# Kernel optimization log

Hardware: AMD Instinct MI355X
Metric: run time of the kernel (lower is better)

Reference implementation:

```python
import jax, jax.numpy as jnp
from jax import lax
import numpy as np

B = 128      # graphs
L = 128      # nodes (tokens) per graph
N = B * L    # total nodes
E = 262144   # edges (avg degree 16)
VOCAB = 50000
EMB = 300
H = 256      # lstm hidden per direction
GCN = 512
NCLS = 2
EPS = 1e-12


def lstm_dir(x, wih, whh, b, reverse):
    # x: [B, L, EMB]; wih: [4H, EMB]; whh: [4H, H]; b: [4H]
    bsz, seq, _ = x.shape
    hdim = whh.shape[1]
    xs = jnp.einsum('ble,ge->blg', x, wih) + b  # [B, L, 4H]
    if reverse:
        xs = xs[:, ::-1]
    def step(carry, xt):
        h, c = carry
        gates = xt + h @ whh.T
        i, f, g, o = jnp.split(gates, 4, axis=-1)  # torch gate order i,f,g,o
        i = jax.nn.sigmoid(i); f = jax.nn.sigmoid(f)
        g = jnp.tanh(g); o = jax.nn.sigmoid(o)
        c = f * c + i * g
        h = o * jnp.tanh(c)
        return (h, c), h
    h0 = jnp.zeros((bsz, hdim), x.dtype)
    _, hs = lax.scan(step, (h0, h0), jnp.swapaxes(xs, 0, 1))
    hs = jnp.swapaxes(hs, 0, 1)  # [B, L, H]
    if reverse:
        hs = hs[:, ::-1]
    return hs


def sage_conv(x, src, dst, Wl, bl, Wr):
    # PyG SAGEConv(mean, normalize=True): lin_l(mean_j x_j) + lin_r(x_i), then L2-normalize
    msg = x[src]                                              # [E, d] gather
    agg = jax.ops.segment_sum(msg, dst, num_segments=x.shape[0])
    cnt = jax.ops.segment_sum(jnp.ones((src.shape[0], 1), x.dtype), dst,
                              num_segments=x.shape[0])
    agg = agg / jnp.maximum(cnt, 1.0)
    out = agg @ Wl + bl + x @ Wr
    nrm = jnp.linalg.norm(out, axis=-1, keepdims=True)
    return out / jnp.maximum(nrm, EPS)


def setup_inputs() -> dict:
    key = jax.random.key(0)
    ks = jax.random.split(key, 24)
    word_seq = jax.random.randint(ks[0], (B, L), 0, VOCAB)
    # intra-graph edges: local endpoints + graph offset
    el = jax.random.randint(ks[1], (2, E), 0, L)
    gid = jnp.repeat(jnp.arange(E // (E // B) * 0 + B), E // B)  # [E]
    edge_index = el + gid[None, :] * L
    batch = jnp.repeat(jnp.arange(B), L)
    s = 0.05
    inp = {
        'word_seq': word_seq, 'edge_index': edge_index, 'batch': batch,
        'embed_table': jax.random.normal(ks[2], (VOCAB, EMB), jnp.float32) * 0.1,
        'wih_f': jax.random.normal(ks[3], (4 * H, EMB), jnp.float32) * s,
        'whh_f': jax.random.normal(ks[4], (4 * H, H), jnp.float32) * s,
        'b_f': jax.random.normal(ks[5], (4 * H,), jnp.float32) * s,
        'wih_b': jax.random.normal(ks[6], (4 * H, EMB), jnp.float32) * s,
        'whh_b': jax.random.normal(ks[7], (4 * H, H), jnp.float32) * s,
        'b_b': jax.random.normal(ks[8], (4 * H,), jnp.float32) * s,
        'Wl1': jax.random.normal(ks[9], (2 * H, GCN), jnp.float32) * s,
        'Wr1': jax.random.normal(ks[10], (2 * H, GCN), jnp.float32) * s,
        'b1': jnp.zeros((GCN,), jnp.float32),
        'Wl2': jax.random.normal(ks[11], (GCN, 512), jnp.float32) * s,
        'Wr2': jax.random.normal(ks[12], (GCN, 512), jnp.float32) * s,
        'b2': jnp.zeros((512,), jnp.float32),
        'Wl3': jax.random.normal(ks[13], (512, 512), jnp.float32) * s,
        'Wr3': jax.random.normal(ks[14], (512, 512), jnp.float32) * s,
        'b3': jnp.zeros((512,), jnp.float32),
        'Wlin': jax.random.normal(ks[15], (512, NCLS), jnp.float32) * s,
        'blin': jnp.zeros((NCLS,), jnp.float32),
    }
    return inp


def reference(word_seq, edge_index, batch, embed_table,
              wih_f, whh_f, b_f, wih_b, whh_b, b_b,
              Wl1, Wr1, b1, Wl2, Wr2, b2, Wl3, Wr3, b3, Wlin, blin):
    # embedding (frozen) over padded per-graph sequences; uniform lengths -> plain reshape
    xe = embed_table[word_seq]                       # [B, L, EMB]
    hf = lstm_dir(xe, wih_f, whh_f, b_f, reverse=False)
    hb = lstm_dir(xe, wih_b, whh_b, b_b, reverse=True)
    x = jnp.concatenate([hf, hb], axis=-1).reshape(N, 2 * H)  # node features
    src, dst = edge_index[0], edge_index[1]
    x = jax.nn.relu(sage_conv(x, src, dst, Wl1, b1, Wr1))
    x = jax.nn.relu(sage_conv(x, src, dst, Wl2, b2, Wr2))
    x = jax.nn.relu(sage_conv(x, src, dst, Wl3, b3, Wr3))
    # global mean pool over graphs
    s = jax.ops.segment_sum(x, batch, num_segments=B)
    c = jax.ops.segment_sum(jnp.ones((N, 1), x.dtype), batch, num_segments=B)
    pooled = s / jnp.maximum(c, 1.0)
    return pooled @ Wlin + blin                      # [B, NCLS]
```

## Files before the change

kernel.cpp:

```cpp
#include <hip/hip_runtime.h>
#include <math.h>

#define NN   16384
#define EE   262144

typedef __attribute__((ext_vector_type(8))) short  short8v;
typedef __attribute__((ext_vector_type(4))) float  f32x4;

__device__ inline unsigned short f2bf(float f) {
    union { float f; unsigned u; } v; v.f = f;
    unsigned r = v.u + 0x7fff + ((v.u >> 16) & 1);
    return (unsigned short)(r >> 16);
}
__device__ inline float bf2f(unsigned short b) {
    unsigned u = ((unsigned)b) << 16;
    union { unsigned u; float f; } v; v.u = u; return v.f;
}
__device__ inline float sigm_f(float x) { return 1.f / (1.f + __expf(-x)); }
__device__ inline float tanh_f(float x) {
    x = fminf(15.f, fmaxf(-15.f, x));
    float e = __expf(2.f * x);
    return (e - 1.f) / (e + 1.f);
}
__device__ inline int gate_orig2(int np) {
    int Q = np >> 8, wv = (np >> 5) & 7, tile = (np >> 4) & 1, tc = np & 15;
    int g = tile * 2 + (tc >> 3);
    int j = Q * 64 + wv * 8 + (tc & 7);
    return g * 256 + j;
}

__device__ __forceinline__ void gload16(const unsigned short* g, unsigned short* l) {
    __builtin_amdgcn_global_load_lds(
        (const __attribute__((address_space(1))) void*)g,
        (__attribute__((address_space(3))) void*)l,
        16, 0, 0);
}

__global__ void k_init(unsigned long long* __restrict__ hx, int* __restrict__ deg,
                       int* __restrict__ fill) {
    int i = blockIdx.x * 256 + threadIdx.x;
    if (i < 65536) hx[i] = 0ull;
    if (i < NN) { deg[i] = 0; fill[i] = 0; }
}

__global__ void k_embed_bf(const int* __restrict__ wseq, const float* __restrict__ tab,
                           unsigned short* __restrict__ xeb) {
    int i = blockIdx.x * 256 + threadIdx.x;
    if (i >= NN * 320) return;
    int row = i / 320, k = i - row * 320;
    float f = (k < 300) ? tab[wseq[row] * 300 + k] : 0.f;
    xeb[i] = f2bf(f);
}

__global__ void k_cvt_wih(const float* __restrict__ wih, unsigned short* __restrict__ wt) {
    int i = blockIdx.x * 256 + threadIdx.x;
    if (i >= 1024 * 320) return;
    int np = i / 320, k = i - np * 320;
    wt[i] = f2bf(k < 300 ? wih[gate_orig2(np) * 300 + k] : 0.f);
}
__global__ void k_cvt_whh(const float* __restrict__ whh, unsigned short* __restrict__ wp) {
    int i = blockIdx.x * 256 + threadIdx.x;
    if (i >= 1024 * 256) return;
    int np = i >> 8, k = i & 255;
    wp[i] = f2bf(whh[gate_orig2(np) * 256 + k]);
}
__global__ void k_permb(const float* __restrict__ b, float* __restrict__ pb) {
    int i = blockIdx.x * 256 + threadIdx.x;
    if (i < 1024) pb[i] = b[gate_orig2(i)];
}
__global__ void k_cvt_wcat(const float* __restrict__ Wl, const float* __restrict__ Wr,
                           unsigned short* __restrict__ wc) {
    int i = blockIdx.x * 256 + threadIdx.x;
    if (i >= 512 * 1024) return;
    int n = i >> 10, k = i & 1023;
    float f = (k < 512) ? Wl[k * 512 + n] : Wr[(k - 512) * 512 + n];
    wc[i] = f2bf(f);
}

__global__ __launch_bounds__(256)
void k_mgemm(const unsigned short* __restrict__ A, const unsigned short* __restrict__ Bt,
             const float* __restrict__ bias, float* __restrict__ C, int N, int Ka)
{
    __shared__ __align__(16) unsigned short As[128 * 32];
    __shared__ __align__(16) unsigned short Bs[128 * 32];
    const int tid = threadIdx.x;
    const int m0 = blockIdx.x << 7, n0 = blockIdx.y << 7;
    const int w = tid >> 6, lane = tid & 63;
    const int wr = w >> 1, wc = w & 1;
    const int lr = lane & 15, lhi = lane >> 4;
    const int rA  = w * 16 + (lane >> 2);
    const int kcA = (lane & 3) * 8;

    const unsigned short* gA0 = A  + (size_t)(m0 + rA) * Ka + kcA;
    const unsigned short* gA1 = gA0 + (size_t)64 * Ka;
    const unsigned short* gB0 = Bt + (size_t)(n0 + rA) * Ka + kcA;
    const unsigned short* gB1 = gB0 + (size_t)64 * Ka;
    unsigned short* lA0 = As + w * 512;
    unsigned short* lA1 = As + 64 * 32 + w * 512;
    unsigned short* lB0 = Bs + w * 512;
    unsigned short* lB1 = Bs + 64 * 32 + w * 512;

    f32x4 acc[4][4] = {};

    for (int k0 = 0; k0 < Ka; k0 += 32) {
        gload16(gA0 + k0, lA0);
        gload16(gA1 + k0, lA1);
        gload16(gB0 + k0, lB0);
        gload16(gB1 + k0, lB1);
        asm volatile("s_waitcnt vmcnt(0)" ::: "memory");
        __syncthreads();
        short8v af[4], bf[4];
        #pragma unroll
        for (int i = 0; i < 4; ++i)
            af[i] = *(const short8v*)&As[(wr * 64 + i * 16 + lr) * 32 + lhi * 8];
        #pragma unroll
        for (int j = 0; j < 4; ++j)
            bf[j] = *(const short8v*)&Bs[(wc * 64 + j * 16 + lr) * 32 + lhi * 8];
        #pragma unroll
        for (int i = 0; i < 4; ++i)
            #pragma unroll
            for (int j = 0; j < 4; ++j)
                acc[i][j] = __builtin_amdgcn_mfma_f32_16x16x32_bf16(af[i], bf[j], acc[i][j], 0, 0, 0);
        __syncthreads();
    }
    #pragma unroll
    for (int i = 0; i < 4; ++i) {
        int row = m0 + wr * 64 + i * 16 + lhi * 4;
        #pragma unroll
        for (int j = 0; j < 4; ++j) {
            int col = n0 + wc * 64 + j * 16 + lr;
            float bv = bias[col];
            #pragma unroll
            for (int r = 0; r < 4; ++r)
                C[(row + r) * N + col] = acc[i][j][r] + bv;
        }
    }
}

__global__ __launch_bounds__(512, 2)
void k_lstm(const float* __restrict__ xs_f, const float* __restrict__ xs_b,
            const unsigned short* __restrict__ whhp_f, const unsigned short* __restrict__ whhp_b,
            unsigned short* __restrict__ xout, unsigned long long* __restrict__ hx)
{
    const int tid  = threadIdx.x;
    const int wv   = tid >> 6, lane = tid & 63;
    const int lr16 = lane & 15, lh = lane >> 4;
    const int b3   = (lane >> 3) & 1, lr3 = lane & 7;
    const int wgid = blockIdx.x;
    const int dir  = wgid >> 5;
    const int bs   = (wgid >> 2) & 7;
    const int Q    = wgid & 3;
    const int b0   = bs * 16;
    const float* xs = dir ? xs_b : xs_f;
    const unsigned short* whhp = dir ? whhp_b : whhp_f;

    const int ncol0 = Q * 256 + wv * 32 + lr16;
    short8v wf[2][8];
    #pragma unroll
    for (int tt = 0; tt < 2; ++tt)
        #pragma unroll
        for (int ks = 0; ks < 8; ++ks)
            wf[tt][ks] = *(const short8v*)(whhp
                + (size_t)(ncol0 + tt * 16) * 256 + ks * 32 + lh * 8);

    __shared__ unsigned short At[2][16 * 256];

    const int grpbase = (dir * 8 + bs) * 4 * 1024;
    unsigned long long* hx_own = hx + grpbase + Q * 1024;

    const int jmine = Q * 64 + wv * 8 + lr3;
    const int rowb  = 4 * lh;
    const int myr0  = rowb + 2 * b3;
    const int up_jl = (tid >> 6) * 8 + (tid & 7);
    const int up_r0 = 2 * ((tid >> 3) & 7);

    float c0 = 0.f, c1 = 0.f;
    float xv0[4], xv1[4];
    {
        const int l0 = dir ? 127 : 0;
        #pragma unroll
        for (int r = 0; r < 4; ++r) {
            const float* xp = xs + ((size_t)(b0 + rowb + r) * 128 + l0) * 1024;
            xv0[r] = xp[ncol0];
            xv1[r] = xp[ncol0 + 16];
        }
    }

    for (int t = 0; t < 128; ++t) {
        const int l = dir ? (127 - t) : t;
        f32x4 acc0 = {}, acc1 = {};
        if (t > 0) {
            const char* Ab = (const char*)&At[(t - 1) & 1][0];
            #pragma unroll
            for (int ks = 0; ks < 8; ++ks) {
                int off = (lr16 * 512 + ks * 64 + lh * 16) ^ ((lr16 & 7) << 4);
                short8v a = *(const short8v*)(Ab + off);
                acc0 = __builtin_amdgcn_mfma_f32_16x16x32_bf16(a, wf[0][ks], acc0, 0, 0, 0);
                acc1 = __builtin_amdgcn_mfma_f32_16x16x32_bf16(a, wf[1][ks], acc1, 0, 0, 0);
            }
        }
        #pragma unroll
        for (int r = 0; r < 4; ++r) { acc0[r] += xv0[r]; acc1[r] += xv1[r]; }
        float z0 = b3 ? acc0[0] : acc0[2];
        float z1 = b3 ? acc0[1] : acc0[3];
        float z2 = b3 ? acc1[0] : acc1[2];
        float z3 = b3 ? acc1[1] : acc1[3];
        float y0 = __shfl_xor(z0, 8);
        float y1 = __shfl_xor(z1, 8);
        float y2 = __shfl_xor(z2, 8);
        float y3 = __shfl_xor(z3, 8);
        float iv0 = b3 ? y0 : acc0[0], iv1 = b3 ? y1 : acc0[1];
        float fv0 = b3 ? acc0[2] : y0, fv1 = b3 ? acc0[3] : y1;
        float gv0 = b3 ? y2 : acc1[0], gv1 = b3 ? y3 : acc1[1];
        float ov0 = b3 ? acc1[2] : y2, ov1 = b3 ? acc1[3] : y3;
        iv0 = sigm_f(iv0); fv0 = sigm_f(fv0); gv0 = tanh_f(gv0); ov0 = sigm_f(ov0);
        c0 = fv0 * c0 + iv0 * gv0;
        float h0 = ov0 * tanh_f(c0);
        iv1 = sigm_f(iv1); fv1 = sigm_f(fv1); gv1 = tanh_f(gv1); ov1 = sigm_f(ov1);
        c1 = fv1 * c1 + iv1 * gv1;
        float h1 = ov1 * tanh_f(c1);
        unsigned short hb0 = f2bf(h0), hb1 = f2bf(h1);
        xout[((size_t)(b0 + myr0)     * 128 + l) * 512 + dir * 256 + jmine] = hb0;
        xout[((size_t)(b0 + myr0 + 1) * 128 + l) * 512 + dir * 256 + jmine] = hb1;

        if (t < 127) {
            const int p = t & 1;
            char* Aw = (char*)&At[p][0];
            {
                int r0_ = myr0, r1_ = myr0 + 1;
                *(unsigned short*)(Aw + ((r0_ * 512 + 2 * jmine) ^ ((r0_ & 7) << 4))) = hb0;
                *(unsigned short*)(Aw + ((r1_ * 512 + 2 * jmine) ^ ((r1_ & 7) << 4))) = hb1;
            }
            const unsigned tg = (unsigned)(t + 1);
            unsigned long long w = ((unsigned long long)tg << 32)
                                 | ((unsigned)hb0 | ((unsigned)hb1 << 16));
            __hip_atomic_store(hx_own + p * 512 + tid, w,
                               __ATOMIC_RELAXED, __HIP_MEMORY_SCOPE_AGENT);
            const int l2 = dir ? (126 - t) : (t + 1);
            #pragma unroll
            for (int r = 0; r < 4; ++r) {
                const float* xp = xs + ((size_t)(b0 + rowb + r) * 128 + l2) * 1024;
                xv0[r] = xp[ncol0];
                xv1[r] = xp[ncol0 + 16];
            }
            const unsigned long long* pp1 = hx + grpbase + (Q ^ 1) * 1024 + p * 512 + tid;
            const unsigned long long* pp2 = hx + grpbase + (Q ^ 2) * 1024 + p * 512 + tid;
            const unsigned long long* pp3 = hx + grpbase + (Q ^ 3) * 1024 + p * 512 + tid;
            unsigned long long u1 = __hip_atomic_load(pp1, __ATOMIC_RELAXED, __HIP_MEMORY_SCOPE_AGENT);
            unsigned long long u2 = __hip_atomic_load(pp2, __ATOMIC_RELAXED, __HIP_MEMORY_SCOPE_AGENT);
            unsigned long long u3 = __hip_atomic_load(pp3, __ATOMIC_RELAXED, __HIP_MEMORY_SCOPE_AGENT);
            while ((unsigned)(u1 >> 32) != tg)
                u1 = __hip_atomic_load(pp1, __ATOMIC_RELAXED, __HIP_MEMORY_SCOPE_AGENT);
            while ((unsigned)(u2 >> 32) != tg)
                u2 = __hip_atomic_load(pp2, __ATOMIC_RELAXED, __HIP_MEMORY_SCOPE_AGENT);
            while ((unsigned)(u3 >> 32) != tg)
                u3 = __hip_atomic_load(pp3, __ATOMIC_RELAXED, __HIP_MEMORY_SCOPE_AGENT);
            {
                int ra = up_r0, rb = up_r0 + 1;
                int j1 = (Q ^ 1) * 64 + up_jl;
                int j2 = (Q ^ 2) * 64 + up_jl;
                int j3 = (Q ^ 3) * 64 + up_jl;
                *(unsigned short*)(Aw + ((ra * 512 + 2 * j1) ^ ((ra & 7) << 4))) =
                    (unsigned short)(u1 & 0xffff);
                *(unsigned short*)(Aw + ((rb * 512 + 2 * j1) ^ ((rb & 7) << 4))) =
                    (unsigned short)((u1 >> 16) & 0xffff);
                *(unsigned short*)(Aw + ((ra * 512 + 2 * j2) ^ ((ra & 7) << 4))) =
                    (unsigned short)(u2 & 0xffff);
                *(unsigned short*)(Aw + ((rb * 512 + 2 * j2) ^ ((rb & 7) << 4))) =
                    (unsigned short)((u2 >> 16) & 0xffff);
                *(unsigned short*)(Aw + ((ra * 512 + 2 * j3) ^ ((ra & 7) << 4))) =
                    (unsigned short)(u3 & 0xffff);
                *(unsigned short*)(Aw + ((rb * 512 + 2 * j3) ^ ((rb & 7) << 4))) =
                    (unsigned short)((u3 >> 16) & 0xffff);
            }
            __syncthreads();
        }
    }
}

__global__ void k_hist(const int* __restrict__ ei, int* __restrict__ deg) {
    int e = blockIdx.x * 256 + threadIdx.x;
    if (e >= EE) return;
    atomicAdd(&deg[ei[EE + e]], 1);
}

__global__ void k_scan(const int* __restrict__ deg, int* __restrict__ indptr) {
    __shared__ int sm[256];
    int tid = threadIdx.x;
    int b0 = tid * 64;
    int s = 0;
    for (int i = 0; i < 64; ++i) s += deg[b0 + i];
    sm[tid] = s;
    __syncthreads();
    for (int off = 1; off < 256; off <<= 1) {
        int v = (tid >= off) ? sm[tid - off] : 0;
        __syncthreads();
        sm[tid] += v;
        __syncthreads();
    }
    int run = sm[tid] - s;
    for (int i = 0; i < 64; ++i) { indptr[b0 + i] = run; run += deg[b0 + i]; }
    if (tid == 255) indptr[NN] = run;
}

__global__ void k_scatter(const int* __restrict__ ei, const int* __restrict__ indptr,
                          int* __restrict__ fill, int* __restrict__ cols) {
    int e = blockIdx.x * 256 + threadIdx.x;
    if (e >= EE) return;
    int d = ei[EE + e];
    int slot = atomicAdd(&fill[d], 1);
    cols[indptr[d] + slot] = ei[e];
}

__global__ __launch_bounds__(512)
void k_gather_lds(const unsigned short* __restrict__ x, const int* __restrict__ indptr,
                  const int* __restrict__ cols, unsigned short* __restrict__ catb)
{
    extern __shared__ char gsm[];
    unsigned short* Xs = (unsigned short*)gsm;
    const int tid  = threadIdx.x;
    const int g    = blockIdx.x >> 1;
    const int hf   = blockIdx.x & 1;
    const int base = g * 128;
    {
        const unsigned short* src = x + (size_t)base * 512;
        #pragma unroll
        for (int it = 0; it < 16; ++it) {
            int i = it * 512 + tid;
            int row = i >> 6, c = (i & 63) * 8;
            *(short8v*)(Xs + row * 512 + c) = *(const short8v*)(src + (size_t)row * 512 + c);
        }
    }
    __syncthreads();
    const int wv = tid >> 6, lane = tid & 63;
    for (int rr = 0; rr < 8; ++rr) {
        int node = base + hf * 64 + rr * 8 + wv;
        int s = indptr[node], e = indptr[node + 1];
        float a[8] = {};
        for (int p = s; p < e; ++p) {
            int lrow = cols[p] - base;
            short8v v = *(const short8v*)(Xs + lrow * 512 + lane * 8);
            #pragma unroll
            for (int q = 0; q < 8; ++q) a[q] += bf2f((unsigned short)v[q]);
        }
        float sc = 1.f / (float)((e - s) > 1 ? (e - s) : 1);
        unsigned short o[8];
        #pragma unroll
        for (int q = 0; q < 8; ++q) o[q] = f2bf(a[q] * sc);
        unsigned short* cp = catb + (size_t)node * 1024 + lane * 8;
        *(short8v*)cp = *(short8v*)o;
        *(short8v*)(cp + 512) = *(const short8v*)(Xs + (node - base) * 512 + lane * 8);
    }
}

__global__ __launch_bounds__(256)
void k_norm_relu_bf(const float* __restrict__ y, unsigned short* __restrict__ o)
{
    int gw = (blockIdx.x * 256 + threadIdx.x) >> 6;
    int lane = threadIdx.x & 63;
    if (gw >= NN) return;
    const float* row = y + gw * 512 + lane * 8;
    float4 v0 = *(const float4*)row;
    float4 v1 = *(const float4*)(row + 4);
    float ss = v0.x*v0.x + v0.y*v0.y + v0.z*v0.z + v0.w*v0.w
             + v1.x*v1.x + v1.y*v1.y + v1.z*v1.z + v1.w*v1.w;
    #pragma unroll
    for (int off = 32; off >= 1; off >>= 1) ss += __shfl_xor(ss, off);
    float sc = 1.f / fmaxf(sqrtf(ss), 1e-12f);
    unsigned short ob[8];
    ob[0] = f2bf(fmaxf(v0.x*sc, 0.f)); ob[1] = f2bf(fmaxf(v0.y*sc, 0.f));
    ob[2] = f2bf(fmaxf(v0.z*sc, 0.f)); ob[3] = f2bf(fmaxf(v0.w*sc, 0.f));
    ob[4] = f2bf(fmaxf(v1.x*sc, 0.f)); ob[5] = f2bf(fmaxf(v1.y*sc, 0.f));
    ob[6] = f2bf(fmaxf(v1.z*sc, 0.f)); ob[7] = f2bf(fmaxf(v1.w*sc, 0.f));
    *(short8v*)(o + gw * 512 + lane * 8) = *(short8v*)ob;
}

__global__ __launch_bounds__(256)
void k_pool_bf(const unsigned short* __restrict__ x, const float* __restrict__ Wlin,
               const float* __restrict__ blin, float* __restrict__ out)
{
    int g = blockIdx.x;
    int tid = threadIdx.x;
    const unsigned short* base = x + (size_t)g * 128 * 512;
    float a0 = 0.f, a1 = 0.f;
    for (int r = 0; r < 128; ++r) {
        unsigned v = *(const unsigned*)(base + r * 512 + 2 * tid);
        a0 += bf2f((unsigned short)(v & 0xffff));
        a1 += bf2f((unsigned short)(v >> 16));
    }
    __shared__ float pooled[512];
    pooled[2*tid]     = a0 * (1.f / 128.f);
    pooled[2*tid + 1] = a1 * (1.f / 128.f);
    __syncthreads();
    if (tid < 64) {
        float p0 = 0.f, p1 = 0.f;
        for (int k = tid; k < 512; k += 64) {
            float pv = pooled[k];
            p0 += pv * Wlin[2*k];
            p1 += pv * Wlin[2*k + 1];
        }
        #pragma unroll
        for (int off = 32; off >= 1; off >>= 1) {
            p0 += __shfl_xor(p0, off);
            p1 += __shfl_xor(p1, off);
        }
        if (tid == 0) {
            out[2*g]     = p0 + blin[0];
            out[2*g + 1] = p1 + blin[1];
        }
    }
}

extern "C" void kernel_launch(void* const* d_in, const int* in_sizes, int n_in,
                              void* d_out, int out_size, void* d_ws, size_t ws_size,
                              hipStream_t stream)
{
    (void)in_sizes; (void)n_in; (void)out_size; (void)ws_size;
    const int*   word_seq = (const int*)  d_in[0];
    const int*   ei       = (const int*)  d_in[1];
    const float* tab      = (const float*)d_in[3];
    const float* wih_f    = (const float*)d_in[4];
    const float* whh_f    = (const float*)d_in[5];
    const float* b_f      = (const float*)d_in[6];
    const float* wih_b    = (const float*)d_in[7];
    const float* whh_b    = (const float*)d_in[8];
    const float* b_b      = (const float*)d_in[9];
    const float* Wl1      = (const float*)d_in[10];
    const float* Wr1      = (const float*)d_in[11];
    const float* b1       = (const float*)d_in[12];
    const float* Wl2      = (const float*)d_in[13];
    const float* Wr2      = (const float*)d_in[14];
    const float* b2       = (const float*)d_in[15];
    const float* Wl3      = (const float*)d_in[16];
    const float* Wr3      = (const float*)d_in[17];
    const float* b3       = (const float*)d_in[18];
    const float* Wlin     = (const float*)d_in[19];
    const float* blin     = (const float*)d_in[20];
    float* out = (float*)d_out;

    char* w = (char*)d_ws;
    int*   deg    = (int*)  (w);
    int*   indptr = (int*)  (w + 65536);
    int*   fill   = (int*)  (w + 131584);
    int*   cols   = (int*)  (w + 197120);
    unsigned long long* hx = (unsigned long long*)(w + 1245696);
    unsigned short* whhp_f = (unsigned short*)(w + 1769984);
    unsigned short* whhp_b = (unsigned short*)(w + 2294272);
    float* pb_f   = (float*)(w + 2818560);
    float* pb_b   = (float*)(w + 2822656);
    unsigned short* wt_f = (unsigned short*)(w + 2826752);
    unsigned short* wt_b = (unsigned short*)(w + 3482112);
    unsigned short* wc1  = (unsigned short*)(w + 4137472);
    unsigned short* wc2  = (unsigned short*)(w + 5186048);
    unsigned short* wc3  = (unsigned short*)(w + 6234624);
    unsigned short* xeb  = (unsigned short*)(w + 7283200);
    float* xs_f   = (float*)(w + 17768960);
    float* xs_b   = (float*)(w + 84877824);
    unsigned short* x0b = (unsigned short*)(w + 151986688);
    unsigned short* catb = (unsigned short*)(w + 17768960);
    float* x1     = (float*)(w + 51323392);
    unsigned short* xb_a = (unsigned short*)(w + 84877824);
    unsigned short* xb_b = (unsigned short*)(w + 101655040);

    k_embed_bf<<<20480, 256, 0, stream>>>(word_seq, tab, xeb);
    k_cvt_wih<<<1280, 256, 0, stream>>>(wih_f, wt_f);
    k_cvt_wih<<<1280, 256, 0, stream>>>(wih_b, wt_b);
    k_cvt_whh<<<1024, 256, 0, stream>>>(whh_f, whhp_f);
    k_cvt_whh<<<1024, 256, 0, stream>>>(whh_b, whhp_b);
    k_permb<<<4, 256, 0, stream>>>(b_f, pb_f);
    k_permb<<<4, 256, 0, stream>>>(b_b, pb_b);
    k_cvt_wcat<<<2048, 256, 0, stream>>>(Wl1, Wr1, wc1);
    k_cvt_wcat<<<2048, 256, 0, stream>>>(Wl2, Wr2, wc2);
    k_cvt_wcat<<<2048, 256, 0, stream>>>(Wl3, Wr3, wc3);

    k_init<<<256, 256, 0, stream>>>(hx, deg, fill);
    k_hist<<<1024, 256, 0, stream>>>(ei, deg);
    k_scan<<<1, 256, 0, stream>>>(deg, indptr);
    k_scatter<<<1024, 256, 0, stream>>>(ei, indptr, fill, cols);

    k_mgemm<<<dim3(128, 8), 256, 0, stream>>>(xeb, wt_f, pb_f, xs_f, 1024, 320);
    k_mgemm<<<dim3(128, 8), 256, 0, stream>>>(xeb, wt_b, pb_b, xs_b, 1024, 320);

    k_lstm<<<64, 512, 0, stream>>>(xs_f, xs_b, whhp_f, whhp_b, x0b, hx);

    k_gather_lds<<<256, 512, 131072, stream>>>(x0b, indptr, cols, catb);
    k_mgemm<<<dim3(128, 4), 256, 0, stream>>>(catb, wc1, b1, x1, 512, 1024);
    k_norm_relu_bf<<<4096, 256, 0, stream>>>(x1, xb_a);
    k_gather_lds<<<256, 512, 131072, stream>>>(xb_a, indptr, cols, catb);
    k_mgemm<<<dim3(128, 4), 256, 0, stream>>>(catb, wc2, b2, x1, 512, 1024);
    k_norm_relu_bf<<<4096, 256, 0, stream>>>(x1, xb_b);
    k_gather_lds<<<256, 512, 131072, stream>>>(xb_b, indptr, cols, catb);
    k_mgemm<<<dim3(128, 4), 256, 0, stream>>>(catb, wc3, b3, x1, 512, 1024);
    k_norm_relu_bf<<<4096, 256, 0, stream>>>(x1, xb_a);

    k_pool_bf<<<128, 256, 0, stream>>>(xb_a, Wlin, blin, out);
}
```

Measured before the change: 649.9 us.

## Interleave two batch slices per LSTM workgroup to hide cross-block exchange latency

Each LSTM workgroup now handles two 16-row batch slices instead of one, so the grid is halved from 64 to 32 blocks. The slices run staggered, and one slice's cross-quarter hidden-state exchange through global atomics overlaps with the other slice's MFMA and gate math. The goal is to hide the spin-wait and global-memory round-trip latency that dominates each recurrent step. In exchange, half as many CUs are used and per-block serial work doubles, so the gain depends on how much of each step was latency rather than compute.

Measured after the change: 810.9 us. 24.8% more time.

```diff
diff --git a/kernel.cpp b/kernel.cpp
--- a/kernel.cpp
+++ b/kernel.cpp
@@ -147,10 +147,10 @@
     const int lr16 = lane & 15, lh = lane >> 4;
     const int b3   = (lane >> 3) & 1, lr3 = lane & 7;
     const int wgid = blockIdx.x;
-    const int dir  = wgid >> 5;
-    const int bs   = (wgid >> 2) & 7;
+    const int dir  = wgid >> 4;
+    const int bp   = (wgid >> 2) & 3;
     const int Q    = wgid & 3;
-    const int b0   = bs * 16;
+    const int b0s0 = bp * 32, b0s1 = bp * 32 + 16;
     const float* xs = dir ? xs_b : xs_f;
     const unsigned short* whhp = dir ? whhp_b : whhp_f;
 
@@ -163,118 +163,200 @@
             wf[tt][ks] = *(const short8v*)(whhp
                 + (size_t)(ncol0 + tt * 16) * 256 + ks * 32 + lh * 8);
 
-    __shared__ unsigned short At[2][16 * 256];
-
-    const int grpbase = (dir * 8 + bs) * 4 * 1024;
-    unsigned long long* hx_own = hx + grpbase + Q * 1024;
+    __shared__ unsigned short At[2][2][16 * 256];
+
+    const int grpQ = (dir * 4 + bp) * 4;
+    unsigned long long* hx_own = hx + (size_t)(grpQ + Q) * 2048;
+    const unsigned long long* hx_p1 = hx + (size_t)(grpQ + (Q ^ 1)) * 2048;
+    const unsigned long long* hx_p2 = hx + (size_t)(grpQ + (Q ^ 2)) * 2048;
+    const unsigned long long* hx_p3 = hx + (size_t)(grpQ + (Q ^ 3)) * 2048;
 
     const int jmine = Q * 64 + wv * 8 + lr3;
     const int rowb  = 4 * lh;
     const int myr0  = rowb + 2 * b3;
     const int up_jl = (tid >> 6) * 8 + (tid & 7);
     const int up_r0 = 2 * ((tid >> 3) & 7);
-
-    float c0 = 0.f, c1 = 0.f;
-    float xv0[4], xv1[4];
+    const int j1 = (Q ^ 1) * 64 + up_jl;
+    const int j2 = (Q ^ 2) * 64 + up_jl;
+    const int j3 = (Q ^ 3) * 64 + up_jl;
+
+    float c0a = 0.f, c1a = 0.f;
+    float c0b = 0.f, c1b = 0.f;
+    float xva0[4], xva1[4], xvb0[4], xvb1[4];
     {
         const int l0 = dir ? 127 : 0;
         #pragma unroll
         for (int r = 0; r < 4; ++r) {
-            const float* xp = xs + ((size_t)(b0 + rowb + r) * 128 + l0) * 1024;
-            xv0[r] = xp[ncol0];
-            xv1[r] = xp[ncol0 + 16];
+            const float* xpa = xs + ((size_t)(b0s0 + rowb + r) * 128 + l0) * 1024;
+            const float* xpb = xs + ((size_t)(b0s1 + rowb + r) * 128 + l0) * 1024;
+            xva0[r] = xpa[ncol0]; xva1[r] = xpa[ncol0 + 16];
+            xvb0[r] = xpb[ncol0]; xvb1[r] = xpb[ncol0 + 16];
         }
     }
 
     for (int t = 0; t < 128; ++t) {
-        const int l = dir ? (127 - t) : t;
-        f32x4 acc0 = {}, acc1 = {};
-        if (t > 0) {
-            const char* Ab = (const char*)&At[(t - 1) & 1][0];
+        const int l  = dir ? (127 - t) : t;
+        const int l2 = dir ? (126 - t) : (t + 1);
+        const int p  = t & 1, q = p ^ 1;
+        const unsigned tg  = (unsigned)t;
+        const unsigned tg1 = (unsigned)(t + 1);
+
+        {
+            f32x4 acc0 = {}, acc1 = {};
+            if (t > 0) {
+                const char* Ab = (const char*)&At[0][q][0];
+                #pragma unroll
+                for (int ks = 0; ks < 8; ++ks) {
+                    int off = (lr16 * 512 + ks * 64 + lh * 16) ^ ((lr16 & 7) << 4);
+                    short8v a = *(const short8v*)(Ab + off);
+                    acc0 = __builtin_amdgcn_mfma_f32_16x16x32_bf16(a, wf[0][ks], acc0, 0, 0, 0);
+                    acc1 = __builtin_amdgcn_mfma_f32_16x16x32_bf16(a, wf[1][ks], acc1, 0, 0, 0);
+                }
+            }
             #pragma unroll
-            for (int ks = 0; ks < 8; ++ks) {
-                int off = (lr16 * 512 + ks * 64 + lh * 16) ^ ((lr16 & 7) << 4);
-                short8v a = *(const short8v*)(Ab + off);
-                acc0 = __builtin_amdgcn_mfma_f32_16x16x32_bf16(a, wf[0][ks], acc0, 0, 0, 0);
-                acc1 = __builtin_amdgcn_mfma_f32_16x16x32_bf16(a, wf[1][ks], acc1, 0, 0, 0);
-            }
-        }
-        #pragma unroll
-        for (int r = 0; r < 4; ++r) { acc0[r] += xv0[r]; acc1[r] += xv1[r]; }
-        float z0 = b3 ? acc0[0] : acc0[2];
-        float z1 = b3 ? acc0[1] : acc0[3];
-        float z2 = b3 ? acc1[0] : acc1[2];
-        float z3 = b3 ? acc1[1] : acc1[3];
-        float y0 = __shfl_xor(z0, 8);
-        float y1 = __shfl_xor(z1, 8);
-        float y2 = __shfl_xor(z2, 8);
-        float y3 = __shfl_xor(z3, 8);
-        float iv0 = b3 ? y0 : acc0[0], iv1 = b3 ? y1 : acc0[1];
-        float fv0 = b3 ? acc0[2] : y0, fv1 = b3 ? acc0[3] : y1;
-        float gv0 = b3 ? y2 : acc1[0], gv1 = b3 ? y3 : acc1[1];
-        float ov0 = b3 ? acc1[2] : y2, ov1 = b3 ? acc1[3] : y3;
-        iv0 = sigm_f(iv0); fv0 = sigm_f(fv0); gv0 = tanh_f(gv0); ov0 = sigm_f(ov0);
-        c0 = fv0 * c0 + iv0 * gv0;
-        float h0 = ov0 * tanh_f(c0);
-        iv1 = sigm_f(iv1); fv1 = sigm_f(fv1); gv1 = tanh_f(gv1); ov1 = sigm_f(ov1);
-        c1 = fv1 * c1 + iv1 * gv1;
-        float h1 = ov1 * tanh_f(c1);
-        unsigned short hb0 = f2bf(h0), hb1 = f2bf(h1);
-        xout[((size_t)(b0 + myr0)     * 128 + l) * 512 + dir * 256 + jmine] = hb0;
-        xout[((size_t)(b0 + myr0 + 1) * 128 + l) * 512 + dir * 256 + jmine] = hb1;
-
-        if (t < 127) {
-            const int p = t & 1;
-            char* Aw = (char*)&At[p][0];
-            {
+            for (int r = 0; r < 4; ++r) { acc0[r] += xva0[r]; acc1[r] += xva1[r]; }
+            float z0 = b3 ? acc0[0] : acc0[2];
+            float z1 = b3 ? acc0[1] : acc0[3];
+            float z2 = b3 ? acc1[0] : acc1[2];
+            float z3 = b3 ? acc1[1] : acc1[3];
+            float y0 = __shfl_xor(z0, 8);
+            float y1 = __shfl_xor(z1, 8);
+            float y2 = __shfl_xor(z2, 8);
+            float y3 = __shfl_xor(z3, 8);
+            float iv0 = b3 ? y0 : acc0[0], iv1 = b3 ? y1 : acc0[1];
+            float fv0 = b3 ? acc0[2] : y0, fv1 = b3 ? acc0[3] : y1;
+            float gv0 = b3 ? y2 : acc1[0], gv1 = b3 ? y3 : acc1[1];
+            float ov0 = b3 ? acc1[2] : y2, ov1 = b3 ? acc1[3] : y3;
+            iv0 = sigm_f(iv0); fv0 = sigm_f(fv0); gv0 = tanh_f(gv0); ov0 = sigm_f(ov0);
+            c0a = fv0 * c0a + iv0 * gv0;
+            float h0 = ov0 * tanh_f(c0a);
+            iv1 = sigm_f(iv1); fv1 = sigm_f(fv1); gv1 = tanh_f(gv1); ov1 = sigm_f(ov1);
+            c1a = fv1 * c1a + iv1 * gv1;
+            float h1 = ov1 * tanh_f(c1a);
+            unsigned short hb0 = f2bf(h0), hb1 = f2bf(h1);
+            xout[((size_t)(b0s0 + myr0)     * 128 + l) * 512 + dir * 256 + jmine] = hb0;
+            xout[((size_t)(b0s0 + myr0 + 1) * 128 + l) * 512 + dir * 256 + jmine] = hb1;
+            if (t < 127) {
+                char* Aw = (char*)&At[0][p][0];
                 int r0_ = myr0, r1_ = myr0 + 1;
                 *(unsigned short*)(Aw + ((r0_ * 512 + 2 * jmine) ^ ((r0_ & 7) << 4))) = hb0;
                 *(unsigned short*)(Aw + ((r1_ * 512 + 2 * jmine) ^ ((r1_ & 7) << 4))) = hb1;
+                unsigned long long w = ((unsigned long long)tg1 << 32)
+                                     | ((unsigned)hb0 | ((unsigned)hb1 << 16));
+                __hip_atomic_store(hx_own + (0 * 2 + p) * 512 + tid, w,
+                                   __ATOMIC_RELAXED, __HIP_MEMORY_SCOPE_AGENT);
+                #pragma unroll
+                for (int r = 0; r < 4; ++r) {
+                    const float* xp = xs + ((size_t)(b0s0 + rowb + r) * 128 + l2) * 1024;
+                    xva0[r] = xp[ncol0]; xva1[r] = xp[ncol0 + 16];
+                }
             }
-            const unsigned tg = (unsigned)(t + 1);
-            unsigned long long w = ((unsigned long long)tg << 32)
-                                 | ((unsigned)hb0 | ((unsigned)hb1 << 16));
-            __hip_atomic_store(hx_own + p * 512 + tid, w,
-                               __ATOMIC_RELAXED, __HIP_MEMORY_SCOPE_AGENT);
-            const int l2 = dir ? (126 - t) : (t + 1);
+        }
+        if (t > 0) {
+            const int so = (1 * 2 + q) * 512 + tid;
+            unsigned long long u1 = __hip_atomic_load(hx_p1 + so, __ATOMIC_RELAXED, __HIP_MEMORY_SCOPE_AGENT);
+            unsigned long long u2 = __hip_atomic_load(hx_p2 + so, __ATOMIC_RELAXED, __HIP_MEMORY_SCOPE_AGENT);
+            unsigned long long u3 = __hip_atomic_load(hx_p3 + so, __ATOMIC_RELAXED, __HIP_MEMORY_SCOPE_AGENT);
+            while ((unsigned)(u1 >> 32) != tg)
+                u1 = __hip_atomic_load(hx_p1 + so, __ATOMIC_RELAXED, __HIP_MEMORY_SCOPE_AGENT);
+            while ((unsigned)(u2 >> 32) != tg)
+                u2 = __hip_atomic_load(hx_p2 + so, __ATOMIC_RELAXED, __HIP_MEMORY_SCOPE_AGENT);
+            while ((unsigned)(u3 >> 32) != tg)
+                u3 = __hip_atomic_load(hx_p3 + so, __ATOMIC_RELAXED, __HIP_MEMORY_SCOPE_AGENT);
+            char* Aw = (char*)&At[1][q][0];
+            int ra = up_r0, rb = up_r0 + 1;
+            *(unsigned short*)(Aw + ((ra * 512 + 2 * j1) ^ ((ra & 7) << 4))) =
+                (unsigned short)(u1 & 0xffff);
+            *(unsigned short*)(Aw + ((rb * 512 + 2 * j1) ^ ((rb & 7) << 4))) =
+                (unsigned short)((u1 >> 16) & 0xffff);
+            *(unsigned short*)(Aw + ((ra * 512 + 2 * j2) ^ ((ra & 7) << 4))) =
+                (unsigned short)(u2 & 0xffff);
+            *(unsigned short*)(Aw + ((rb * 512 + 2 * j2) ^ ((rb & 7) << 4))) =
+                (unsigned short)((u2 >> 16) & 0xffff);
+            *(unsigned short*)(Aw + ((ra * 512 + 2 * j3) ^ ((ra & 7) << 4))) =
+                (unsigned short)(u3 & 0xffff);
+            *(unsigned short*)(Aw + ((rb * 512 + 2 * j3) ^ ((rb & 7) << 4))) =
+                (unsigned short)((u3 >> 16) & 0xffff);
+        }
+        __syncthreads();
+        {
+            f32x4 acc0 = {}, acc1 = {};
+            if (t > 0) {
+                const char* Ab = (const char*)&At[1][q][0];
+                #pragma unroll
+                for (int ks = 0; ks < 8; ++ks) {
+                    int off = (lr16 * 512 + ks * 64 + lh * 16) ^ ((lr16 & 7) << 4);
+                    short8v a = *(const short8v*)(Ab + off);
+                    acc0 = __builtin_amdgcn_mfma_f32_16x16x32_bf16(a, wf[0][ks], acc0, 0, 0, 0);
+                    acc1 = __builtin_amdgcn_mfma_f32_16x16x32_bf16(a, wf[1][ks], acc1, 0, 0, 0);
+                }
+            }
             #pragma unroll
-            for (int r = 0; r < 4; ++r) {
-                const float* xp = xs + ((size_t)(b0 + rowb + r) * 128 + l2) * 1024;
-                xv0[r] = xp[ncol0];
-                xv1[r] = xp[ncol0 + 16];
+            for (int r = 0; r < 4; ++r) { acc0[r] += xvb0[r]; acc1[r] += xvb1[r]; }
+            float z0 = b3 ? acc0[0] : acc0[2];
+            float z1 = b3 ? acc0[1] : acc0[3];
+            float z2 = b3 ? acc1[0] : acc1[2];
+            float z3 = b3 ? acc1[1] : acc1[3];
+            float y0 = __shfl_xor(z0, 8);
+            float y1 = __shfl_xor(z1, 8);
+            float y2 = __shfl_xor(z2, 8);
+            float y3 = __shfl_xor(z3, 8);
+            float iv0 = b3 ? y0 : acc0[0], iv1 = b3 ? y1 : acc0[1];
+            float fv0 = b3 ? acc0[2] : y0, fv1 = b3 ? acc0[3] : y1;
+            float gv0 = b3 ? y2 : acc1[0], gv1 = b3 ? y3 : acc1[1];
+            float ov0 = b3 ? acc1[2] : y2, ov1 = b3 ? acc1[3] : y3;
+            iv0 = sigm_f(iv0); fv0 = sigm_f(fv0); gv0 = tanh_f(gv0); ov0 = sigm_f(ov0);
+            c0b = fv0 * c0b + iv0 * gv0;
+            float h0 = ov0 * tanh_f(c0b);
+            iv1 = sigm_f(iv1); fv1 = sigm_f(fv1); gv1 = tanh_f(gv1); ov1 = sigm_f(ov1);
+            c1b = fv1 * c1b + iv1 * gv1;
+            float h1 = ov1 * tanh_f(c1b);
+            unsigned short hb0 = f2bf(h0), hb1 = f2bf(h1);
+            xout[((size_t)(b0s1 + myr0)     * 128 + l) * 512 + dir * 256 + jmine] = hb0;
+            xout[((size_t)(b0s1 + myr0 + 1) * 128 + l) * 512 + dir * 256 + jmine] = hb1;
+            if (t < 127) {
+                char* Aw = (char*)&At[1][p][0];
+                int r0_ = myr0, r1_ = myr0 + 1;
+                *(unsigned short*)(Aw + ((r0_ * 512 + 2 * jmine) ^ ((r0_ & 7) << 4))) = hb0;
+                *(unsigned short*)(Aw + ((r1_ * 512 + 2 * jmine) ^ ((r1_ & 7) << 4))) = hb1;
+                unsigned long long w = ((unsigned long long)tg1 << 32)
+                                     | ((unsigned)hb0 | ((unsigned)hb1 << 16));
+                __hip_atomic_store(hx_own + (1 * 2 + p) * 512 + tid, w,
+                                   __ATOMIC_RELAXED, __HIP_MEMORY_SCOPE_AGENT);
+                #pragma unroll
+                for (int r = 0; r < 4; ++r) {
+                    const float* xp = xs + ((size_t)(b0s1 + rowb + r) * 128 + l2) * 1024;
+                    xvb0[r] = xp[ncol0]; xvb1[r] = xp[ncol0 + 16];
+                }
             }
-            const unsigned long long* pp1 = hx + grpbase + (Q ^ 1) * 1024 + p * 512 + tid;
-            const unsigned long long* pp2 = hx + grpbase + (Q ^ 2) * 1024 + p * 512 + tid;
-            const unsigned long long* pp3 = hx + grpbase + (Q ^ 3) * 1024 + p * 512 + tid;
-            unsigned long long u1 = __hip_atomic_load(pp1, __ATOMIC_RELAXED, __HIP_MEMORY_SCOPE_AGENT);
-            unsigned long long u2 = __hip_atomic_load(pp2, __ATOMIC_RELAXED, __HIP_MEMORY_SCOPE_AGENT);
-            unsigned long long u3 = __hip_atomic_load(pp3, __ATOMIC_RELAXED, __HIP_MEMORY_SCOPE_AGENT);
-            while ((unsigned)(u1 >> 32) != tg)
-                u1 = __hip_atomic_load(pp1, __ATOMIC_RELAXED, __HIP_MEMORY_SCOPE_AGENT);
-            while ((unsigned)(u2 >> 32) != tg)
-                u2 = __hip_atomic_load(pp2, __ATOMIC_RELAXED, __HIP_MEMORY_SCOPE_AGENT);
-            while ((unsigned)(u3 >> 32) != tg)
-                u3 = __hip_atomic_load(pp3, __ATOMIC_RELAXED, __HIP_MEMORY_SCOPE_AGENT);
-            {
-                int ra = up_r0, rb = up_r0 + 1;
-                int j1 = (Q ^ 1) * 64 + up_jl;
-                int j2 = (Q ^ 2) * 64 + up_jl;
-                int j3 = (Q ^ 3) * 64 + up_jl;
-                *(unsigned short*)(Aw + ((ra * 512 + 2 * j1) ^ ((ra & 7) << 4))) =
-                    (unsigned short)(u1 & 0xffff);
-                *(unsigned short*)(Aw + ((rb * 512 + 2 * j1) ^ ((rb & 7) << 4))) =
-                    (unsigned short)((u1 >> 16) & 0xffff);
-                *(unsigned short*)(Aw + ((ra * 512 + 2 * j2) ^ ((ra & 7) << 4))) =
-                    (unsigned short)(u2 & 0xffff);
-                *(unsigned short*)(Aw + ((rb * 512 + 2 * j2) ^ ((rb & 7) << 4))) =
-                    (unsigned short)((u2 >> 16) & 0xffff);
-                *(unsigned short*)(Aw + ((ra * 512 + 2 * j3) ^ ((ra & 7) << 4))) =
-                    (unsigned short)(u3 & 0xffff);
-                *(unsigned short*)(Aw + ((rb * 512 + 2 * j3) ^ ((rb & 7) << 4))) =
-                    (unsigned short)((u3 >> 16) & 0xffff);
-            }
-            __syncthreads();
-        }
+        }
+        if (t < 127) {
+            const int so = (0 * 2 + p) * 512 + tid;
+            unsigned long long u1 = __hip_atomic_load(hx_p1 + so, __ATOMIC_RELAXED, __HIP_MEMORY_SCOPE_AGENT);
+            unsigned long long u2 = __hip_atomic_load(hx_p2 + so, __ATOMIC_RELAXED, __HIP_MEMORY_SCOPE_AGENT);
+            unsigned long long u3 = __hip_atomic_load(hx_p3 + so, __ATOMIC_RELAXED, __HIP_MEMORY_SCOPE_AGENT);
+            while ((unsigned)(u1 >> 32) != tg1)
+                u1 = __hip_atomic_load(hx_p1 + so, __ATOMIC_RELAXED, __HIP_MEMORY_SCOPE_AGENT);
+            while ((unsigned)(u2 >> 32) != tg1)
+                u2 = __hip_atomic_load(hx_p2 + so, __ATOMIC_RELAXED, __HIP_MEMORY_SCOPE_AGENT);
+            while ((unsigned)(u3 >> 32) != tg1)
+                u3 = __hip_atomic_load(hx_p3 + so, __ATOMIC_RELAXED, __HIP_MEMORY_SCOPE_AGENT);
+            char* Aw = (char*)&At[0][p][0];
+            int ra = up_r0, rb = up_r0 + 1;
+            *(unsigned short*)(Aw + ((ra * 512 + 2 * j1) ^ ((ra & 7) << 4))) =
+                (unsigned short)(u1 & 0xffff);
+            *(unsigned short*)(Aw + ((rb * 512 + 2 * j1) ^ ((rb & 7) << 4))) =
+                (unsigned short)((u1 >> 16) & 0xffff);
+            *(unsigned short*)(Aw + ((ra * 512 + 2 * j2) ^ ((ra & 7) << 4))) =
+                (unsigned short)(u2 & 0xffff);
+            *(unsigned short*)(Aw + ((rb * 512 + 2 * j2) ^ ((rb & 7) << 4))) =
+                (unsigned short)((u2 >> 16) & 0xffff);
+            *(unsigned short*)(Aw + ((ra * 512 + 2 * j3) ^ ((ra & 7) << 4))) =
+                (unsigned short)(u3 & 0xffff);
+            *(unsigned short*)(Aw + ((rb * 512 + 2 * j3) ^ ((rb & 7) << 4))) =
+                (unsigned short)((u3 >> 16) & 0xffff);
+        }
+        __syncthreads();
     }
 }
 
@@ -481,7 +563,7 @@
     k_mgemm<<<dim3(128, 8), 256, 0, stream>>>(xeb, wt_f, pb_f, xs_f, 1024, 320);
     k_mgemm<<<dim3(128, 8), 256, 0, stream>>>(xeb, wt_b, pb_b, xs_b, 1024, 320);
 
-    k_lstm<<<64, 512, 0, stream>>>(xs_f, xs_b, whhp_f, whhp_b, x0b, hx);
+    k_lstm<<<32, 512, 0, stream>>>(xs_f, xs_b, whhp_f, whhp_b, x0b, hx);
 
     k_gather_lds<<<256, 512, 131072, stream>>>(x0b, indptr, cols, catb);
     k_mgemm<<<dim3(128, 4), 256, 0, stream>>>(catb, wc1, b1, x1, 512, 1024);
```
